# Kernel optimization log

Measured on AMD Instinct MI355X. Metric: run time of the kernel, lower is better.

Reference implementation:

```python
import jax, jax.numpy as jnp
from jax import lax
import numpy as np

D_MODEL = 128
N_HEADS = 8
N_POINTS = 8
MAX_MAG = 10.0
NEG_SLOPE = 0.1


def conv2d(x, w, b, pad):
    # x: (N, Cin, H, W), w: (Cout, Cin, kh, kw)
    y = lax.conv_general_dilated(x, w, (1, 1), [(pad, pad), (pad, pad)],
                                 dimension_numbers=('NCHW', 'OIHW', 'NCHW'))
    return y + b[None, :, None, None]


def leaky(x):
    return jnp.where(x >= 0, x, NEG_SLOPE * x)


def bilinear_sample(img, grid):
    # img: (B, C, H, W); grid: (B, P, H, W, 2) in [-1, 1] (x, y)
    # Matches torch F.grid_sample(mode='bilinear', padding_mode='zeros', align_corners=False)
    B, C, H, W = img.shape
    x = ((grid[..., 0] + 1.0) * W - 1.0) * 0.5
    y = ((grid[..., 1] + 1.0) * H - 1.0) * 0.5
    x0 = jnp.floor(x)
    y0 = jnp.floor(y)
    wx1 = x - x0
    wy1 = y - y0

    def one(img_b, x0b, y0b, wx1b, wy1b):
        def gather(xi, yi):
            valid = (xi >= 0) & (xi < W) & (yi >= 0) & (yi < H)
            xc = jnp.clip(xi, 0, W - 1).astype(jnp.int32)
            yc = jnp.clip(yi, 0, H - 1).astype(jnp.int32)
            v = img_b[:, yc, xc]  # (C, P, H, W)
            return v * valid
        wx0b = 1.0 - wx1b
        wy0b = 1.0 - wy1b
        v00 = gather(x0b, y0b)
        v01 = gather(x0b + 1, y0b)
        v10 = gather(x0b, y0b + 1)
        v11 = gather(x0b + 1, y0b + 1)
        return (v00 * (wx0b * wy0b) + v01 * (wx1b * wy0b)
                + v10 * (wx0b * wy1b) + v11 * (wx1b * wy1b))

    return jax.vmap(one)(img, x0, y0, wx1, wy1)  # (B, C, P, H, W)


def ss_deform_attn(value, loc):
    # value: (N, nh, d, H, W); loc: (N, nh, P, H, W, 2) in normalized [0,1] coords
    N, nh, d, H, W = value.shape
    P = loc.shape[2]
    v = value.reshape(N * nh, d, H, W)
    grids = (2.0 * loc - 1.0).reshape(N * nh, P, H, W, 2)
    sampled = bilinear_sample(v, grids)  # (N*nh, d, P, H, W)
    # per-location attention logits = <sampled_point, value_at_location>
    scores = jnp.einsum('ndphw,ndhw->nphw', sampled, v)
    aw = jax.nn.softmax(scores, axis=1)
    out = jnp.einsum('ndphw,nphw->ndhw', sampled, aw)
    return out.reshape(N, nh * d, H, W)


def _forward(query, value, reference_points, co_w1, co_b1, co_w2, co_b2,
             co_w3, co_b3, co_w4, co_b4, val_w, val_b, out_w, out_b):
    N, C, H, W = value.shape
    v = conv2d(value, val_w, val_b, 0)
    v = v.reshape(N, N_HEADS, D_MODEL // N_HEADS, H, W)
    o = leaky(conv2d(query, co_w1, co_b1, 1))
    o = leaky(conv2d(o, co_w2, co_b2, 1))
    o = leaky(conv2d(o, co_w3, co_b3, 1))
    o = conv2d(o, co_w4, co_b4, 1)
    o = MAX_MAG * jnp.tanh(o)
    offsets = o.reshape(N, N_HEADS, N_POINTS, H, W, 2)
    norm = jnp.array([W, H], dtype=o.dtype)  # (x, y) normalizer
    loc = reference_points[:, None, None, :, :, :] + offsets / norm
    out = ss_deform_attn(v, loc)
    return conv2d(out, out_w, out_b, 0)


def setup_inputs() -> dict:
    key = jax.random.key(0)
    ks = jax.random.split(key, 12)
    N, H, W = 4, 80, 80

    def w_init(k, shape):
        fan_in = shape[1] * shape[2] * shape[3]
        return jax.random.normal(k, shape, jnp.float32) / np.sqrt(fan_in)

    return {
        'query': jax.random.normal(ks[0], (N, 2 * D_MODEL, H, W), jnp.float32),
        'value': jax.random.normal(ks[1], (N, D_MODEL, H, W), jnp.float32),
        'reference_points': jax.random.uniform(ks[2], (N, H, W, 2), jnp.float32),
        'co_w1': w_init(ks[3], (D_MODEL, 2 * D_MODEL, 3, 3)),
        'co_b1': jnp.zeros((D_MODEL,), jnp.float32),
        'co_w2': w_init(ks[4], (D_MODEL, D_MODEL, 3, 3)),
        'co_b2': jnp.zeros((D_MODEL,), jnp.float32),
        'co_w3': w_init(ks[5], (D_MODEL, D_MODEL, 3, 3)),
        'co_b3': jnp.zeros((D_MODEL,), jnp.float32),
        'co_w4': w_init(ks[6], (N_HEADS * N_POINTS * 2, D_MODEL, 3, 3)),
        'co_b4': jnp.zeros((N_HEADS * N_POINTS * 2,), jnp.float32),
        'val_w': w_init(ks[7], (D_MODEL, D_MODEL, 1, 1)),
        'val_b': jnp.zeros((D_MODEL,), jnp.float32),
        'out_w': w_init(ks[8], (D_MODEL, D_MODEL, 1, 1)),
        'out_b': jnp.zeros((D_MODEL,), jnp.float32),
    }


def reference(query, value, reference_points, co_w1, co_b1, co_w2, co_b2,
              co_w3, co_b3, co_w4, co_b4, val_w, val_b, out_w, out_b):
    return _forward(query, value, reference_points, co_w1, co_b1, co_w2, co_b2,
                    co_w3, co_b3, co_w4, co_b4, val_w, val_b, out_w, out_b)
```

## Files before the change

### kernel.cpp

```cpp
#include <hip/hip_runtime.h>
#include <math.h>

#define Hh 80
#define Ww 80
#define HW 6400
#define PS 6724
#define NB 4

typedef _Float16 half8 __attribute__((ext_vector_type(8)));
typedef _Float16 half4v __attribute__((ext_vector_type(4)));
typedef float f32x16 __attribute__((ext_vector_type(16)));

__device__ __forceinline__ void gload16(const _Float16* g, _Float16* l) {
    __builtin_amdgcn_global_load_lds(
        (const __attribute__((address_space(1))) void*)g,
        (__attribute__((address_space(3))) void*)l, 16, 0, 0);
}

__device__ inline void wblob_one(const float* src, _Float16* dst, int CI, int d) {
    int NC = CI / 32;
    int j = d & 7;
    int l = (d >> 3) & 63;
    int h = (d >> 9) & 1;
    int rest = d >> 10;
    int tap = rest % 9;
    rest /= 9;
    int c = rest % NC;
    int CT = rest / NC;
    int co = CT * 32 + (l & 31);
    int ci = c * 32 + h * 16 + (l >> 5) * 8 + j;
    dst[d] = (_Float16)src[((size_t)co * CI + ci) * 9 + tap];
}

__device__ inline void wblob1x1_one(const float* src, _Float16* dst, int d) {
    int j = d & 7;
    int l = (d >> 3) & 63;
    int c = (d >> 9) & 7;
    int CT = d >> 12;
    int co = CT * 32 + (l & 31);
    int ci = c * 16 + (l >> 5) * 8 + j;
    dst[d] = (_Float16)src[co * 128 + ci];
}

__device__ inline int padsite(int p) {
    if (p < 82) return p;
    if (p < 164) return 81 * 82 + (p - 82);
    if (p < 244) return (p - 163) * 82;
    return (p - 243) * 82 + 81;
}

__global__ void prep_kernel(const float* __restrict__ w1, const float* __restrict__ w2,
                            const float* __restrict__ w3, const float* __restrict__ w4,
                            const float* __restrict__ vw, const float* __restrict__ ow,
                            _Float16* __restrict__ b1, _Float16* __restrict__ b2,
                            _Float16* __restrict__ b3, _Float16* __restrict__ b4,
                            _Float16* __restrict__ bv, _Float16* __restrict__ bo,
                            int* __restrict__ qh_i, int* __restrict__ hA_i,
                            int* __restrict__ hB_i) {
    int idx = blockIdx.x * 256 + threadIdx.x;
    if (idx < 294912) { wblob_one(w1, b1, 256, idx); return; }
    idx -= 294912;
    if (idx < 147456) { wblob_one(w2, b2, 128, idx); return; }
    idx -= 147456;
    if (idx < 147456) { wblob_one(w3, b3, 128, idx); return; }
    idx -= 147456;
    if (idx < 147456) { wblob_one(w4, b4, 128, idx); return; }
    idx -= 147456;
    if (idx < 16384) { wblob1x1_one(vw, bv, idx); return; }
    idx -= 16384;
    if (idx < 16384) { wblob1x1_one(ow, bo, idx); return; }
    idx -= 16384;
    if (idx < 165888) {
        int n = idx / 41472, rr = idx % 41472;
        int c = rr / 5184, r2 = rr % 5184;
        int p = r2 >> 4, k = r2 & 15;
        qh_i[((size_t)(n * 8 + c) * PS + padsite(p)) * 16 + k] = 0;
        return;
    }
    idx -= 165888;
    if (idx < 82944) {
        int n = idx / 20736, rr = idx % 20736;
        int c = rr / 5184, r2 = rr % 5184;
        int p = r2 >> 4, k = r2 & 15;
        hA_i[((size_t)(n * 4 + c) * PS + padsite(p)) * 16 + k] = 0;
        return;
    }
    idx -= 82944;
    if (idx < 82944) {
        int n = idx / 20736, rr = idx % 20736;
        int c = rr / 5184, r2 = rr % 5184;
        int p = r2 >> 4, k = r2 & 15;
        hB_i[((size_t)(n * 4 + c) * PS + padsite(p)) * 16 + k] = 0;
    }
}

__global__ __launch_bounds__(256) void q_transpose(
    const float* __restrict__ in, _Float16* __restrict__ out) {
    const int b = blockIdx.x;
    const int xcd = b & 7, n = xcd & 3, hi = xcd >> 2;
    const int s0 = hi * 3200 + (b >> 3) * 64;
    const int t = threadIdx.x;
    constexpr int CI = 256, ST = CI + 8;
    __shared__ _Float16 T[64 * ST];
    for (int idx = t; idx < 64 * CI; idx += 256) {
        int ci = idx >> 6, sl = idx & 63;
        T[sl * ST + ci] = (_Float16)in[((size_t)n * CI + ci) * HW + s0 + sl];
    }
    __syncthreads();
    for (int idx = t; idx < 64 * 32; idx += 256) {
        int q = idx & 31, sl = idx >> 5;
        int s = s0 + sl, yy = s / 80, xx = s % 80;
        int c = q >> 2, off = (q & 3) * 8;
        *(int4*)(out + ((size_t)(n * 8 + c) * PS + (yy + 1) * 82 + (xx + 1)) * 32 + off) =
            *(const int4*)(&T[sl * ST + q * 8]);
    }
}

__global__ __launch_bounds__(256) void v_transpose(
    const float* __restrict__ in, _Float16* __restrict__ out) {
    const int b = blockIdx.x;
    const int xcd = b & 7, n = xcd & 3, hi = xcd >> 2;
    const int s0 = hi * 3200 + (b >> 3) * 64;
    const int t = threadIdx.x;
    constexpr int CI = 128, ST = CI + 8;
    __shared__ _Float16 T[64 * ST];
    for (int idx = t; idx < 64 * CI; idx += 256) {
        int ci = idx >> 6, sl = idx & 63;
        T[sl * ST + ci] = (_Float16)in[((size_t)n * CI + ci) * HW + s0 + sl];
    }
    __syncthreads();
    for (int idx = t; idx < 64 * 16; idx += 256) {
        int q = idx & 15, sl = idx >> 4;
        *(int4*)(out + ((size_t)n * HW + s0 + sl) * CI + q * 8) =
            *(const int4*)(&T[sl * ST + q * 8]);
    }
}

template <int NCp, int ACT>
__global__ __launch_bounds__(256, 2) void conv3x3_mfma(
    const _Float16* __restrict__ in, const _Float16* __restrict__ wblob,
    const float* __restrict__ bias, void* __restrict__ outp) {
    constexpr int NS = NCp * 18;
    constexpr int NG = NCp * 3;
    __shared__ _Float16 Abuf[2][24 * 512];
    __shared__ _Float16 Bbuf[2][6 * 1024];

    const int b = blockIdx.x;
    const int xcd = b & 7, n = xcd & 3, hi = xcd >> 2;
    const int r = b >> 3;
    const int x0 = (r % 5) * 16, y0 = hi * 40 + (r / 5) * 4;
    const int t = threadIdx.x;
    const int w = t >> 6, l = t & 63;
    const int lane31 = l & 31, lhalf = l >> 5;
    const int lx = lane31 & 15, lyw = lane31 >> 4;
    const int si = l & 15, g8 = l >> 4;

    const _Float16* bplane0 = in + (size_t)(n * NCp) * PS * 32;
    const _Float16* wA = wblob + (size_t)w * NS * 512 + l * 8;

    f32x16 acc0 = {}, acc1 = {};

#pragma unroll
    for (int k2 = 0; k2 < 6; ++k2)
        gload16(wA + (size_t)k2 * 512, &Abuf[0][(k2 * 4 + w) * 512]);
#pragma unroll
    for (int j = 0; j < 3; ++j) {
        const int m = 3 * w + j, rr = m >> 1, sg = m & 1;
        gload16(bplane0 + ((size_t)((y0 + rr) * 82 + x0 + sg * 16 + si)) * 32 + g8 * 8,
                &Bbuf[0][rr * 1024 + sg * 512]);
    }
    __syncthreads();

    const _Float16* bplane = bplane0;
#pragma unroll 1
    for (int c = 0; c < NCp; ++c) {
        const _Float16* bplaneN = bplane + (size_t)PS * 32;
        const int cpar = c & 1;
#pragma unroll
        for (int gi = 0; gi < 3; ++gi) {
            const int grp = c * 3 + gi;
            if (grp + 1 < NG) {
                const _Float16* asrc = wA + (size_t)(grp + 1) * 6 * 512;
                _Float16* adst = &Abuf[(grp + 1) & 1][w * 512];
#pragma unroll
                for (int k2 = 0; k2 < 6; ++k2)
                    gload16(asrc + (size_t)k2 * 512, adst + k2 * 4 * 512);
            }
            if (gi == 2 && c + 1 < NCp) {
#pragma unroll
                for (int j = 0; j < 3; ++j) {
                    const int m = 3 * w + j, rr = m >> 1, sg = m & 1;
                    gload16(bplaneN + ((size_t)((y0 + rr) * 82 + x0 + sg * 16 + si)) * 32 + g8 * 8,
                            &Bbuf[(c + 1) & 1][rr * 1024 + sg * 512]);
                }
            }
            const _Float16* ab = Abuf[grp & 1];
            const _Float16* bb = Bbuf[cpar];
#pragma unroll
            for (int k = 0; k < 6; ++k) {
                const int u = gi * 6 + k;
                const int tap = u >> 1, h = u & 1;
                const int dy = tap / 3, dx = tap % 3;
                half8 a = *(const half8*)&ab[(k * 4 + w) * 512 + l * 8];
                const int cx = lx + dx;
                const int boff = (cx >> 4) * 512 + (h * 2 + lhalf) * 128 + (cx & 15) * 8;
                half8 b0 = *(const half8*)&bb[(lyw + dy) * 1024 + boff];
                half8 b1 = *(const half8*)&bb[(lyw + 2 + dy) * 1024 + boff];
                acc0 = __builtin_amdgcn_mfma_f32_32x32x16_f16(a, b0, acc0, 0, 0, 0);
                acc1 = __builtin_amdgcn_mfma_f32_32x32x16_f16(a, b1, acc1, 0, 0, 0);
            }
            __syncthreads();
        }
        bplane = bplaneN;
    }

    const int x = x0 + lx;
#pragma unroll
    for (int f = 0; f < 2; ++f) {
        const f32x16& acc = f ? acc1 : acc0;
        const int y = y0 + lyw + 2 * f;
#pragma unroll
        for (int q = 0; q < 4; ++q) {
            const int inner = 8 * q + 4 * lhalf;
            const int co0 = w * 32 + inner;
            float v[4];
#pragma unroll
            for (int i = 0; i < 4; ++i) {
                float vv = acc[q * 4 + i] + bias[co0 + i];
                if (ACT == 1) vv = (vv >= 0.f) ? vv : 0.1f * vv;
                else vv = 10.f * tanhf(vv);
                v[i] = vv;
            }
            if (ACT == 1) {
                half4v hv = {(_Float16)v[0], (_Float16)v[1], (_Float16)v[2], (_Float16)v[3]};
                *(half4v*)((_Float16*)outp +
                    ((size_t)(n * 4 + w) * PS + (y + 1) * 82 + (x + 1)) * 32 + inner) = hv;
            } else {
                float4 fv = {v[0], v[1], v[2], v[3]};
                *(float4*)((float*)outp + ((size_t)n * HW + y * 80 + x) * 128 + co0) = fv;
            }
        }
    }
}

template <int MODE>
__global__ __launch_bounds__(256) void conv1x1_mfma(
    const _Float16* __restrict__ in, const _Float16* __restrict__ wblob,
    const float* __restrict__ bias, float* __restrict__ outp) {
    const int b = blockIdx.x;
    const int xcd = b & 7, n = xcd & 3, hi = xcd >> 2;
    const int r = b >> 3;
    const int coH = r & 1, strip = r >> 1;
    const int t = threadIdx.x;
    const int w = t >> 6, l = t & 63;
    const int lane31 = l & 31, lhalf = l >> 5;
    const int s = hi * 3200 + strip * 128 + w * 32 + lane31;

    const _Float16* pB = in + (size_t)(n * HW + s) * 128 + lhalf * 8;
    const _Float16* pA0 = wblob + (size_t)(coH * 2) * 8 * 512 + l * 8;
    const _Float16* pA1 = pA0 + 8 * 512;

    half8 bB[8], bA0[8], bA1[8];
#pragma unroll
    for (int c = 0; c < 8; ++c) {
        bB[c]  = *(const half8*)(pB + c * 16);
        bA0[c] = *(const half8*)(pA0 + (size_t)c * 512);
        bA1[c] = *(const half8*)(pA1 + (size_t)c * 512);
    }
    f32x16 acc0 = {}, acc1 = {};
#pragma unroll
    for (int c = 0; c < 8; ++c) {
        acc0 = __builtin_amdgcn_mfma_f32_32x32x16_f16(bA0[c], bB[c], acc0, 0, 0, 0);
        acc1 = __builtin_amdgcn_mfma_f32_32x32x16_f16(bA1[c], bB[c], acc1, 0, 0, 0);
    }

#pragma unroll
    for (int ct = 0; ct < 2; ++ct) {
        const f32x16& acc = ct ? acc1 : acc0;
#pragma unroll
        for (int q = 0; q < 4; ++q) {
            const int co0 = coH * 64 + ct * 32 + 8 * q + 4 * lhalf;
            if (MODE == 0) {
                const int hd = co0 >> 4, dd = co0 & 15;
                float4 fv = {acc[4 * q + 0] + bias[co0 + 0], acc[4 * q + 1] + bias[co0 + 1],
                             acc[4 * q + 2] + bias[co0 + 2], acc[4 * q + 3] + bias[co0 + 3]};
                *(float4*)&outp[((size_t)(n * 8 + hd) * HW + s) * 16 + dd] = fv;
            } else {
#pragma unroll
                for (int i = 0; i < 4; ++i)
                    outp[(size_t)(n * 128 + co0 + i) * HW + s] = acc[4 * q + i] + bias[co0 + i];
            }
        }
    }
}

__global__ __launch_bounds__(256, 2) void deform_attn_kernel(
    const float* __restrict__ v_s, const float* __restrict__ offs,
    const float* __restrict__ ref, _Float16* __restrict__ att) {
    const int slice = blockIdx.x;
    const int n = slice >> 3, hd = slice & 7;
    const int t = threadIdx.x;
    const int s = blockIdx.y * 64 + (t >> 2);
    const int d0 = (t & 3) * 4;
    const int nb = n * 8 + hd;
    const float* vbase = v_s + (size_t)nb * (HW * 16) + d0;

    const float4 cv = *(const float4*)&v_s[((size_t)nb * HW + s) * 16 + d0];
    const float rx = ref[(size_t)(n * HW + s) * 2 + 0] * 80.f - 0.5f;
    const float ry = ref[(size_t)(n * HW + s) * 2 + 1] * 80.f - 0.5f;

    const int e = (s >= 3200) ? 1 : 0;
    const float* ob0 = offs + ((size_t)n * HW + (2 * s - e * HW)) * 128 + hd * 16 + e;

    float4 oxv[4], oyv[4];
#pragma unroll
    for (int i = 0; i < 4; ++i) {
        oxv[i] = *(const float4*)(ob0 + i * 4);
        oyv[i] = *(const float4*)(ob0 + 128 + i * 4);
    }
    float ox[8], oy[8];
#pragma unroll
    for (int i = 0; i < 4; ++i) {
        ox[2 * i] = oxv[i].x; ox[2 * i + 1] = oxv[i].z;
        oy[2 * i] = oyv[i].x; oy[2 * i + 1] = oyv[i].z;
    }

    float wx1[8], wy1[8];
    int ix[8], iy[8];
#pragma unroll
    for (int p = 0; p < 8; ++p) {
        const float px = rx + ox[p];
        const float py = ry + oy[p];
        const float fx = floorf(px), fy = floorf(py);
        ix[p] = (int)fx; iy[p] = (int)fy;
        wx1[p] = px - fx; wy1[p] = py - fy;
    }

    float4 g[8][4];
#pragma unroll
    for (int p = 0; p < 8; ++p) {
        const int xc0 = min(max(ix[p], 0), 79),     xc1 = min(max(ix[p] + 1, 0), 79);
        const int yc0 = min(max(iy[p], 0), 79),     yc1 = min(max(iy[p] + 1, 0), 79);
        const int r0 = yc0 * 80, r1 = yc1 * 80;
        g[p][0] = *(const float4*)(vbase + (size_t)(r0 + xc0) * 16);
        g[p][1] = *(const float4*)(vbase + (size_t)(r0 + xc1) * 16);
        g[p][2] = *(const float4*)(vbase + (size_t)(r1 + xc0) * 16);
        g[p][3] = *(const float4*)(vbase + (size_t)(r1 + xc1) * 16);
    }

    float4 sampled[8];
    float score[8];
#pragma unroll
    for (int p = 0; p < 8; ++p) {
        const float vx0 = (ix[p] >= 0 && ix[p] < Ww) ? 1.f : 0.f;
        const float vx1 = (ix[p] + 1 >= 0 && ix[p] + 1 < Ww) ? 1.f : 0.f;
        const float vy0 = (iy[p] >= 0 && iy[p] < Hh) ? 1.f : 0.f;
        const float vy1 = (iy[p] + 1 >= 0 && iy[p] + 1 < Hh) ? 1.f : 0.f;
        const float wx0 = 1.f - wx1[p], wy0 = 1.f - wy1[p];
        const float w00 = wx0 * wy0 * vx0 * vy0;
        const float w01 = wx1[p] * wy0 * vx1 * vy0;
        const float w10 = wx0 * wy1[p] * vx0 * vy1;
        const float w11 = wx1[p] * wy1[p] * vx1 * vy1;
        float4 sv;
        sv.x = g[p][0].x * w00 + g[p][1].x * w01 + g[p][2].x * w10 + g[p][3].x * w11;
        sv.y = g[p][0].y * w00 + g[p][1].y * w01 + g[p][2].y * w10 + g[p][3].y * w11;
        sv.z = g[p][0].z * w00 + g[p][1].z * w01 + g[p][2].z * w10 + g[p][3].z * w11;
        sv.w = g[p][0].w * w00 + g[p][1].w * w01 + g[p][2].w * w10 + g[p][3].w * w11;
        sampled[p] = sv;
        float sc = sv.x * cv.x + sv.y * cv.y + sv.z * cv.z + sv.w * cv.w;
        sc += __shfl_xor(sc, 1);
        sc += __shfl_xor(sc, 2);
        score[p] = sc;
    }

    float m = score[0];
#pragma unroll
    for (int p = 1; p < 8; ++p) m = fmaxf(m, score[p]);
    float sum = 0.f, aw[8];
#pragma unroll
    for (int p = 0; p < 8; ++p) {
        aw[p] = __expf(score[p] - m);
        sum += aw[p];
    }
    const float inv = 1.f / sum;
    float4 o = {0.f, 0.f, 0.f, 0.f};
#pragma unroll
    for (int p = 0; p < 8; ++p) {
        o.x += aw[p] * sampled[p].x;
        o.y += aw[p] * sampled[p].y;
        o.z += aw[p] * sampled[p].z;
        o.w += aw[p] * sampled[p].w;
    }
    o.x *= inv; o.y *= inv; o.z *= inv; o.w *= inv;

    half4v hv = {(_Float16)o.x, (_Float16)o.y, (_Float16)o.z, (_Float16)o.w};
    *(half4v*)&att[((size_t)n * HW + s) * 128 + hd * 16 + d0] = hv;
}

extern "C" void kernel_launch(void* const* d_in, const int* in_sizes, int n_in,
                              void* d_out, int out_size, void* d_ws, size_t ws_size,
                              hipStream_t stream) {
    const float* query = (const float*)d_in[0];
    const float* value = (const float*)d_in[1];
    const float* ref   = (const float*)d_in[2];
    const float* co_w1 = (const float*)d_in[3];
    const float* co_b1 = (const float*)d_in[4];
    const float* co_w2 = (const float*)d_in[5];
    const float* co_b2 = (const float*)d_in[6];
    const float* co_w3 = (const float*)d_in[7];
    const float* co_b3 = (const float*)d_in[8];
    const float* co_w4 = (const float*)d_in[9];
    const float* co_b4 = (const float*)d_in[10];
    const float* val_w = (const float*)d_in[11];
    const float* val_b = (const float*)d_in[12];
    const float* out_w = (const float*)d_in[13];
    const float* out_b = (const float*)d_in[14];

    char* ws = (char*)d_ws;
    size_t o = 0;
    auto alloc = [&](size_t bytes) { char* p = ws + o; o += (bytes + 255) & ~(size_t)255; return p; };

    _Float16* wb2 = (_Float16*)alloc(147456 * 2);
    _Float16* wb3 = (_Float16*)alloc(147456 * 2);
    _Float16* wb4 = (_Float16*)alloc(147456 * 2);
    _Float16* wbv = (_Float16*)alloc(16384 * 2);
    _Float16* wbo = (_Float16*)alloc(16384 * 2);
    char* vsR = alloc(3276800 * 4);
    float* v_s = (float*)vsR;
    _Float16* wb1 = (_Float16*)vsR;
    _Float16* v_h = (_Float16*)alloc((size_t)NB * HW * 128 * 2);
    char* R1 = alloc((size_t)NB * 8 * PS * 32 * 2);
    _Float16* q_h = (_Float16*)R1;
    float* o4 = (float*)R1;
    char* R2 = alloc((size_t)NB * 4 * PS * 32 * 2 * 2);
    _Float16* hA = (_Float16*)R2;
    _Float16* hB = (_Float16*)(R2 + (size_t)NB * 4 * PS * 32 * 2);
    _Float16* att_h = (_Float16*)R2;

    prep_kernel<<<4304, 256, 0, stream>>>(co_w1, co_w2, co_w3, co_w4, val_w, out_w,
                                          wb1, wb2, wb3, wb4, wbv, wbo,
                                          (int*)q_h, (int*)hA, (int*)hB);

    q_transpose<<<400, 256, 0, stream>>>(query, q_h);
    v_transpose<<<400, 256, 0, stream>>>(value, v_h);

    conv3x3_mfma<8, 1><<<400, 256, 0, stream>>>(q_h, wb1, co_b1, hA);

    conv1x1_mfma<0><<<400, 256, 0, stream>>>(v_h, wbv, val_b, v_s);

    conv3x3_mfma<4, 1><<<400, 256, 0, stream>>>(hA, wb2, co_b2, hB);
    conv3x3_mfma<4, 1><<<400, 256, 0, stream>>>(hB, wb3, co_b3, hA);
    conv3x3_mfma<4, 2><<<400, 256, 0, stream>>>(hA, wb4, co_b4, o4);

    deform_attn_kernel<<<dim3(32, 100), 256, 0, stream>>>(v_s, o4, ref, att_h);

    conv1x1_mfma<1><<<400, 256, 0, stream>>>(att_h, wbo, out_b, (float*)d_out);
}
```

Before: 238.6 us.

## Use two waves per conv3x3 block, each computing two output-channel tiles

Result: slower. 251.9 us (+5.6%).

```diff
diff --git a/kernel.cpp b/kernel.cpp
--- a/kernel.cpp
+++ b/kernel.cpp
@@ -137,7 +137,7 @@
 }
 
 template <int NCp, int ACT>
-__global__ __launch_bounds__(256, 2) void conv3x3_mfma(
+__global__ __launch_bounds__(128, 1) void conv3x3_mfma(
     const _Float16* __restrict__ in, const _Float16* __restrict__ wblob,
     const float* __restrict__ bias, void* __restrict__ outp) {
     constexpr int NS = NCp * 18;
@@ -156,16 +156,19 @@
     const int si = l & 15, g8 = l >> 4;
 
     const _Float16* bplane0 = in + (size_t)(n * NCp) * PS * 32;
-    const _Float16* wA = wblob + (size_t)w * NS * 512 + l * 8;
-
-    f32x16 acc0 = {}, acc1 = {};
-
-#pragma unroll
-    for (int k2 = 0; k2 < 6; ++k2)
-        gload16(wA + (size_t)k2 * 512, &Abuf[0][(k2 * 4 + w) * 512]);
-#pragma unroll
-    for (int j = 0; j < 3; ++j) {
-        const int m = 3 * w + j, rr = m >> 1, sg = m & 1;
+    const _Float16* wA0 = wblob + (size_t)(2 * w) * NS * 512 + l * 8;
+    const _Float16* wA1 = wA0 + (size_t)NS * 512;
+
+    f32x16 acc00 = {}, acc01 = {}, acc10 = {}, acc11 = {};
+
+#pragma unroll
+    for (int k2 = 0; k2 < 6; ++k2) {
+        gload16(wA0 + (size_t)k2 * 512, &Abuf[0][(k2 * 4 + 2 * w) * 512]);
+        gload16(wA1 + (size_t)k2 * 512, &Abuf[0][(k2 * 4 + 2 * w + 1) * 512]);
+    }
+#pragma unroll
+    for (int j = 0; j < 6; ++j) {
+        const int m = 6 * w + j, rr = m >> 1, sg = m & 1;
         gload16(bplane0 + ((size_t)((y0 + rr) * 82 + x0 + sg * 16 + si)) * 32 + g8 * 8,
                 &Bbuf[0][rr * 1024 + sg * 512]);
     }
@@ -180,16 +183,19 @@
         for (int gi = 0; gi < 3; ++gi) {
             const int grp = c * 3 + gi;
             if (grp + 1 < NG) {
-                const _Float16* asrc = wA + (size_t)(grp + 1) * 6 * 512;
-                _Float16* adst = &Abuf[(grp + 1) & 1][w * 512];
-#pragma unroll
-                for (int k2 = 0; k2 < 6; ++k2)
-                    gload16(asrc + (size_t)k2 * 512, adst + k2 * 4 * 512);
+                const _Float16* a0src = wA0 + (size_t)(grp + 1) * 6 * 512;
+                const _Float16* a1src = wA1 + (size_t)(grp + 1) * 6 * 512;
+                _Float16* adst = &Abuf[(grp + 1) & 1][2 * w * 512];
+#pragma unroll
+                for (int k2 = 0; k2 < 6; ++k2) {
+                    gload16(a0src + (size_t)k2 * 512, adst + (size_t)(k2 * 4) * 512);
+                    gload16(a1src + (size_t)k2 * 512, adst + (size_t)(k2 * 4 + 1) * 512);
+                }
             }
             if (gi == 2 && c + 1 < NCp) {
 #pragma unroll
-                for (int j = 0; j < 3; ++j) {
-                    const int m = 3 * w + j, rr = m >> 1, sg = m & 1;
+                for (int j = 0; j < 6; ++j) {
+                    const int m = 6 * w + j, rr = m >> 1, sg = m & 1;
                     gload16(bplaneN + ((size_t)((y0 + rr) * 82 + x0 + sg * 16 + si)) * 32 + g8 * 8,
                             &Bbuf[(c + 1) & 1][rr * 1024 + sg * 512]);
                 }
@@ -201,13 +207,16 @@
                 const int u = gi * 6 + k;
                 const int tap = u >> 1, h = u & 1;
                 const int dy = tap / 3, dx = tap % 3;
-                half8 a = *(const half8*)&ab[(k * 4 + w) * 512 + l * 8];
+                half8 a0 = *(const half8*)&ab[(k * 4 + 2 * w) * 512 + l * 8];
+                half8 a1 = *(const half8*)&ab[(k * 4 + 2 * w + 1) * 512 + l * 8];
                 const int cx = lx + dx;
                 const int boff = (cx >> 4) * 512 + (h * 2 + lhalf) * 128 + (cx & 15) * 8;
                 half8 b0 = *(const half8*)&bb[(lyw + dy) * 1024 + boff];
                 half8 b1 = *(const half8*)&bb[(lyw + 2 + dy) * 1024 + boff];
-                acc0 = __builtin_amdgcn_mfma_f32_32x32x16_f16(a, b0, acc0, 0, 0, 0);
-                acc1 = __builtin_amdgcn_mfma_f32_32x32x16_f16(a, b1, acc1, 0, 0, 0);
+                acc00 = __builtin_amdgcn_mfma_f32_32x32x16_f16(a0, b0, acc00, 0, 0, 0);
+                acc01 = __builtin_amdgcn_mfma_f32_32x32x16_f16(a0, b1, acc01, 0, 0, 0);
+                acc10 = __builtin_amdgcn_mfma_f32_32x32x16_f16(a1, b0, acc10, 0, 0, 0);
+                acc11 = __builtin_amdgcn_mfma_f32_32x32x16_f16(a1, b1, acc11, 0, 0, 0);
             }
             __syncthreads();
         }
@@ -216,28 +225,32 @@
 
     const int x = x0 + lx;
 #pragma unroll
-    for (int f = 0; f < 2; ++f) {
-        const f32x16& acc = f ? acc1 : acc0;
-        const int y = y0 + lyw + 2 * f;
-#pragma unroll
-        for (int q = 0; q < 4; ++q) {
-            const int inner = 8 * q + 4 * lhalf;
-            const int co0 = w * 32 + inner;
-            float v[4];
-#pragma unroll
-            for (int i = 0; i < 4; ++i) {
-                float vv = acc[q * 4 + i] + bias[co0 + i];
-                if (ACT == 1) vv = (vv >= 0.f) ? vv : 0.1f * vv;
-                else vv = 10.f * tanhf(vv);
-                v[i] = vv;
-            }
-            if (ACT == 1) {
-                half4v hv = {(_Float16)v[0], (_Float16)v[1], (_Float16)v[2], (_Float16)v[3]};
-                *(half4v*)((_Float16*)outp +
-                    ((size_t)(n * 4 + w) * PS + (y + 1) * 82 + (x + 1)) * 32 + inner) = hv;
-            } else {
-                float4 fv = {v[0], v[1], v[2], v[3]};
-                *(float4*)((float*)outp + ((size_t)n * HW + y * 80 + x) * 128 + co0) = fv;
+    for (int a = 0; a < 2; ++a) {
+        const int ct = 2 * w + a;
+#pragma unroll
+        for (int f = 0; f < 2; ++f) {
+            const f32x16& acc = a ? (f ? acc11 : acc10) : (f ? acc01 : acc00);
+            const int y = y0 + lyw + 2 * f;
+#pragma unroll
+            for (int q = 0; q < 4; ++q) {
+                const int inner = 8 * q + 4 * lhalf;
+                const int co0 = ct * 32 + inner;
+                float v[4];
+#pragma unroll
+                for (int i = 0; i < 4; ++i) {
+                    float vv = acc[q * 4 + i] + bias[co0 + i];
+                    if (ACT == 1) vv = (vv >= 0.f) ? vv : 0.1f * vv;
+                    else vv = 10.f * tanhf(vv);
+                    v[i] = vv;
+                }
+                if (ACT == 1) {
+                    half4v hv = {(_Float16)v[0], (_Float16)v[1], (_Float16)v[2], (_Float16)v[3]};
+                    *(half4v*)((_Float16*)outp +
+                        ((size_t)(n * 4 + ct) * PS + (y + 1) * 82 + (x + 1)) * 32 + inner) = hv;
+                } else {
+                    float4 fv = {v[0], v[1], v[2], v[3]};
+                    *(float4*)((float*)outp + ((size_t)n * HW + y * 80 + x) * 128 + co0) = fv;
+                }
             }
         }
     }
@@ -444,13 +457,13 @@
     q_transpose<<<400, 256, 0, stream>>>(query, q_h);
     v_transpose<<<400, 256, 0, stream>>>(value, v_h);
 
-    conv3x3_mfma<8, 1><<<400, 256, 0, stream>>>(q_h, wb1, co_b1, hA);
+    conv3x3_mfma<8, 1><<<400, 128, 0, stream>>>(q_h, wb1, co_b1, hA);
 
     conv1x1_mfma<0><<<400, 256, 0, stream>>>(v_h, wbv, val_b, v_s);
 
-    conv3x3_mfma<4, 1><<<400, 256, 0, stream>>>(hA, wb2, co_b2, hB);
-    conv3x3_mfma<4, 1><<<400, 256, 0, stream>>>(hB, wb3, co_b3, hA);
-    conv3x3_mfma<4, 2><<<400, 256, 0, stream>>>(hA, wb4, co_b4, o4);
+    conv3x3_mfma<4, 1><<<400, 128, 0, stream>>>(hA, wb2, co_b2, hB);
+    conv3x3_mfma<4, 1><<<400, 128, 0, stream>>>(hB, wb3, co_b3, hA);
+    conv3x3_mfma<4, 2><<<400, 128, 0, stream>>>(hA, wb4, co_b4, o4);
 
     deform_attn_kernel<<<dim3(32, 100), 256, 0, stream>>>(v_s, o4, ref, att_h);
 
```

## Use partial vmcnt waits and raw barriers to overlap conv3x3 LDS prefetch

Applied to the files above, without the earlier changes.

New measurement: 234.2 us. No clear change (-1.9%).

```diff
diff --git a/kernel.cpp b/kernel.cpp
--- a/kernel.cpp
+++ b/kernel.cpp
@@ -15,6 +15,14 @@
     __builtin_amdgcn_global_load_lds(
         (const __attribute__((address_space(1))) void*)g,
         (__attribute__((address_space(3))) void*)l, 16, 0, 0);
+}
+
+#define WAITVM(N) asm volatile("s_waitcnt vmcnt(" #N ")" ::: "memory")
+
+__device__ __forceinline__ void barrier_mem() {
+    asm volatile("" ::: "memory");
+    __builtin_amdgcn_s_barrier();
+    asm volatile("" ::: "memory");
 }
 
 __device__ inline void wblob_one(const float* src, _Float16* dst, int CI, int d) {
@@ -141,7 +149,6 @@
     const _Float16* __restrict__ in, const _Float16* __restrict__ wblob,
     const float* __restrict__ bias, void* __restrict__ outp) {
     constexpr int NS = NCp * 18;
-    constexpr int NG = NCp * 3;
     __shared__ _Float16 Abuf[2][24 * 512];
     __shared__ _Float16 Bbuf[2][6 * 1024];
 
@@ -160,58 +167,79 @@
 
     f32x16 acc0 = {}, acc1 = {};
 
-#pragma unroll
-    for (int k2 = 0; k2 < 6; ++k2)
-        gload16(wA + (size_t)k2 * 512, &Abuf[0][(k2 * 4 + w) * 512]);
-#pragma unroll
-    for (int j = 0; j < 3; ++j) {
-        const int m = 3 * w + j, rr = m >> 1, sg = m & 1;
-        gload16(bplane0 + ((size_t)((y0 + rr) * 82 + x0 + sg * 16 + si)) * 32 + g8 * 8,
-                &Bbuf[0][rr * 1024 + sg * 512]);
-    }
-    __syncthreads();
+    auto stageA = [&](int grp) {
+        const _Float16* asrc = wA + (size_t)grp * 6 * 512;
+        _Float16* adst = &Abuf[grp & 1][w * 512];
+#pragma unroll
+        for (int k2 = 0; k2 < 6; ++k2)
+            gload16(asrc + (size_t)k2 * 512, adst + (size_t)(k2 * 4) * 512);
+    };
+    auto stageB = [&](const _Float16* plane, int par) {
+#pragma unroll
+        for (int j = 0; j < 3; ++j) {
+            const int m = 3 * w + j, rr = m >> 1, sg = m & 1;
+            gload16(plane + ((size_t)((y0 + rr) * 82 + x0 + sg * 16 + si)) * 32 + g8 * 8,
+                    &Bbuf[par][rr * 1024 + sg * 512]);
+        }
+    };
+    auto compute6 = [&](int gi, const _Float16* ab, const _Float16* bb) {
+#pragma unroll
+        for (int k = 0; k < 6; ++k) {
+            const int u = gi * 6 + k;
+            const int tap = u >> 1, h = u & 1;
+            const int dy = tap / 3, dx = tap % 3;
+            half8 a = *(const half8*)&ab[(k * 4 + w) * 512 + l * 8];
+            const int cx = lx + dx;
+            const int boff = (cx >> 4) * 512 + (h * 2 + lhalf) * 128 + (cx & 15) * 8;
+            half8 b0 = *(const half8*)&bb[(lyw + dy) * 1024 + boff];
+            half8 b1 = *(const half8*)&bb[(lyw + 2 + dy) * 1024 + boff];
+            acc0 = __builtin_amdgcn_mfma_f32_32x32x16_f16(a, b0, acc0, 0, 0, 0);
+            acc1 = __builtin_amdgcn_mfma_f32_32x32x16_f16(a, b1, acc1, 0, 0, 0);
+        }
+    };
+
+    stageA(0);
+    stageB(bplane0, 0);
 
     const _Float16* bplane = bplane0;
 #pragma unroll 1
-    for (int c = 0; c < NCp; ++c) {
+    for (int c = 0; c < NCp - 1; ++c) {
         const _Float16* bplaneN = bplane + (size_t)PS * 32;
-        const int cpar = c & 1;
-#pragma unroll
-        for (int gi = 0; gi < 3; ++gi) {
-            const int grp = c * 3 + gi;
-            if (grp + 1 < NG) {
-                const _Float16* asrc = wA + (size_t)(grp + 1) * 6 * 512;
-                _Float16* adst = &Abuf[(grp + 1) & 1][w * 512];
-#pragma unroll
-                for (int k2 = 0; k2 < 6; ++k2)
-                    gload16(asrc + (size_t)k2 * 512, adst + k2 * 4 * 512);
-            }
-            if (gi == 2 && c + 1 < NCp) {
-#pragma unroll
-                for (int j = 0; j < 3; ++j) {
-                    const int m = 3 * w + j, rr = m >> 1, sg = m & 1;
-                    gload16(bplaneN + ((size_t)((y0 + rr) * 82 + x0 + sg * 16 + si)) * 32 + g8 * 8,
-                            &Bbuf[(c + 1) & 1][rr * 1024 + sg * 512]);
-                }
-            }
-            const _Float16* ab = Abuf[grp & 1];
-            const _Float16* bb = Bbuf[cpar];
-#pragma unroll
-            for (int k = 0; k < 6; ++k) {
-                const int u = gi * 6 + k;
-                const int tap = u >> 1, h = u & 1;
-                const int dy = tap / 3, dx = tap % 3;
-                half8 a = *(const half8*)&ab[(k * 4 + w) * 512 + l * 8];
-                const int cx = lx + dx;
-                const int boff = (cx >> 4) * 512 + (h * 2 + lhalf) * 128 + (cx & 15) * 8;
-                half8 b0 = *(const half8*)&bb[(lyw + dy) * 1024 + boff];
-                half8 b1 = *(const half8*)&bb[(lyw + 2 + dy) * 1024 + boff];
-                acc0 = __builtin_amdgcn_mfma_f32_32x32x16_f16(a, b0, acc0, 0, 0, 0);
-                acc1 = __builtin_amdgcn_mfma_f32_32x32x16_f16(a, b1, acc1, 0, 0, 0);
-            }
-            __syncthreads();
-        }
+        const _Float16* bb = Bbuf[c & 1];
+        stageA(3 * c + 1);
+        WAITVM(6);
+        barrier_mem();
+        compute6(0, Abuf[(3 * c) & 1], bb);
+        barrier_mem();
+        stageA(3 * c + 2);
+        WAITVM(6);
+        barrier_mem();
+        compute6(1, Abuf[(3 * c + 1) & 1], bb);
+        barrier_mem();
+        stageA(3 * c + 3);
+        stageB(bplaneN, (c + 1) & 1);
+        WAITVM(9);
+        barrier_mem();
+        compute6(2, Abuf[(3 * c + 2) & 1], bb);
+        barrier_mem();
         bplane = bplaneN;
+    }
+    {
+        const int c = NCp - 1;
+        const _Float16* bb = Bbuf[c & 1];
+        stageA(3 * c + 1);
+        WAITVM(6);
+        barrier_mem();
+        compute6(0, Abuf[(3 * c) & 1], bb);
+        barrier_mem();
+        stageA(3 * c + 2);
+        WAITVM(6);
+        barrier_mem();
+        compute6(1, Abuf[(3 * c + 1) & 1], bb);
+        barrier_mem();
+        WAITVM(0);
+        barrier_mem();
+        compute6(2, Abuf[(3 * c + 2) & 1], bb);
     }
 
     const int x = x0 + lx;
```
